# Optimization experiments

Hardware: AMD Instinct MI355X
Metric: run time of the kernel (lower is better)

## Reference

```python
import jax, jax.numpy as jnp
import numpy as np

B, N, IN_DIM = 256, 300, 1280
DIM, DEPTH, HEADS = 256, 2, 4
DIM_HEAD = DIM // HEADS            # 64
NB_FEAT = int(DIM_HEAD * np.log(DIM_HEAD))  # 266, lucidrains default
FF_HIDDEN = 4 * DIM
LN_EPS = 1e-5
KERNEL_EPS = 1e-4


def _orthogonal_random_matrix(nb_rows, nb_cols, rng):
    # gaussian orthogonal random matrix, scaling=0 (chi-norm multipliers)
    blocks = []
    full = nb_rows // nb_cols
    for _ in range(full):
        q, _ = np.linalg.qr(rng.standard_normal((nb_cols, nb_cols)))
        blocks.append(q.T)
    rem = nb_rows - full * nb_cols
    if rem:
        q, _ = np.linalg.qr(rng.standard_normal((nb_cols, nb_cols)))
        blocks.append(q.T[:rem])
    mat = np.concatenate(blocks, 0)
    mult = np.linalg.norm(rng.standard_normal((nb_rows, nb_cols)), axis=1)
    return (mult[:, None] * mat).astype(np.float32)


def setup_inputs() -> dict:
    key = jax.random.key(0)
    ks = jax.random.split(key, 24)
    s = 0.02
    rng = np.random.default_rng(0)
    proj = jnp.asarray(np.stack([_orthogonal_random_matrix(NB_FEAT, DIM_HEAD, rng)
                                 for _ in range(DEPTH)]))  # [L, M, dh]
    return {
        "x": jax.random.normal(ks[0], (B, N, IN_DIM), jnp.float32),
        "w_in": jax.random.normal(ks[1], (IN_DIM, DIM), jnp.float32) * s,
        "b_in": jnp.zeros((DIM,), jnp.float32),
        "proj": proj,
        "ln1_g": jnp.ones((DEPTH, DIM), jnp.float32),
        "ln1_b": jnp.zeros((DEPTH, DIM), jnp.float32),
        "wq": jax.random.normal(ks[2], (DEPTH, DIM, DIM), jnp.float32) * s,
        "wk": jax.random.normal(ks[3], (DEPTH, DIM, DIM), jnp.float32) * s,
        "wv": jax.random.normal(ks[4], (DEPTH, DIM, DIM), jnp.float32) * s,
        "wo": jax.random.normal(ks[5], (DEPTH, DIM, DIM), jnp.float32) * s,
        "bo": jnp.zeros((DEPTH, DIM), jnp.float32),
        "ln2_g": jnp.ones((DEPTH, DIM), jnp.float32),
        "ln2_b": jnp.zeros((DEPTH, DIM), jnp.float32),
        "w1": jax.random.normal(ks[6], (DEPTH, DIM, FF_HIDDEN), jnp.float32) * s,
        "b1": jnp.zeros((DEPTH, FF_HIDDEN), jnp.float32),
        "w2": jax.random.normal(ks[7], (DEPTH, FF_HIDDEN, DIM), jnp.float32) * s,
        "b2": jnp.zeros((DEPTH, DIM), jnp.float32),
        "hln_g": jnp.ones((DIM,), jnp.float32),
        "hln_b": jnp.zeros((DIM,), jnp.float32),
        "wh1": jax.random.normal(ks[8], (DIM, 128), jnp.float32) * s,
        "bh1": jnp.zeros((128,), jnp.float32),
        "wh2": jax.random.normal(ks[9], (128, 1), jnp.float32) * s,
        "bh2": jnp.zeros((1,), jnp.float32),
    }


def _layernorm(x, g, b):
    mu = jnp.mean(x, -1, keepdims=True)
    var = jnp.mean(jnp.square(x - mu), -1, keepdims=True)
    return (x - mu) * jax.lax.rsqrt(var + LN_EPS) * g + b


def _softmax_kernel(data, proj, is_query):
    # data: [b,h,n,dh], proj: [m,dh] -> features [b,h,n,m] (FAVOR+ positive softmax kernel)
    norm = DIM_HEAD ** -0.25
    ratio = proj.shape[0] ** -0.5
    dd = jnp.einsum('bhnd,md->bhnm', data * norm, proj)
    diag = 0.5 * jnp.sum(jnp.square(data), -1) * (norm ** 2)  # [b,h,n]
    if is_query:
        stab = jnp.max(dd, axis=-1, keepdims=True)
    else:
        stab = jnp.max(dd, axis=(-2, -1), keepdims=True)
    return ratio * (jnp.exp(dd - diag[..., None] - stab) + KERNEL_EPS)


def _linear_attention(q, k, v, proj):
    # non-causal FAVOR+: O(n*m*d) instead of O(n^2*d)
    qp = _softmax_kernel(q, proj, True)    # [b,h,n,m]
    kp = _softmax_kernel(k, proj, False)   # [b,h,n,m]
    d_inv = 1.0 / jnp.einsum('bhnm,bhm->bhn', qp, jnp.sum(kp, axis=-2))
    context = jnp.einsum('bhnm,bhnd->bhmd', kp, v)
    return jnp.einsum('bhnm,bhmd->bhnd', qp, context) * d_inv[..., None]


def reference(x, w_in, b_in, proj, ln1_g, ln1_b, wq, wk, wv, wo, bo,
              ln2_g, ln2_b, w1, b1, w2, b2, hln_g, hln_b, wh1, bh1, wh2, bh2):
    h = x @ w_in + b_in                                   # [B,N,DIM]
    for l in range(DEPTH):
        # --- pre-norm FAVOR+ self-attention ---
        y = _layernorm(h, ln1_g[l], ln1_b[l])
        q = (y @ wq[l]).reshape(B, N, HEADS, DIM_HEAD).transpose(0, 2, 1, 3)
        k = (y @ wk[l]).reshape(B, N, HEADS, DIM_HEAD).transpose(0, 2, 1, 3)
        v = (y @ wv[l]).reshape(B, N, HEADS, DIM_HEAD).transpose(0, 2, 1, 3)
        o = _linear_attention(q, k, v, proj[l])
        o = o.transpose(0, 2, 1, 3).reshape(B, N, DIM)
        h = h + (o @ wo[l] + bo[l])
        # --- pre-norm FFN (GELU, mult=4) ---
        y = _layernorm(h, ln2_g[l], ln2_b[l])
        h = h + (jax.nn.gelu(y @ w1[l] + b1[l]) @ w2[l] + b2[l])
    pooled = jnp.mean(h, axis=1)                          # [B,DIM]
    z = _layernorm(pooled, hln_g, hln_b)
    z = jax.nn.relu(z @ wh1 + bh1)
    return jax.nn.sigmoid(z @ wh2 + bh2)                  # [B,1]
```

## Files before the change

kernel.cpp:

```cpp
#include <hip/hip_runtime.h>
#include <hip/hip_bf16.h>


#define MF 266
#define NSEQ 300
#define DIMC 256
#define NORM_QK 0.3535533905932738f
#define KEPS 1e-4f

typedef __attribute__((ext_vector_type(8))) short bf16x8;
typedef __attribute__((ext_vector_type(4))) float f32x4;

#define MFMA16(a, b, c) __builtin_amdgcn_mfma_f32_16x16x32_bf16((a), (b), (c), 0, 0, 0)

__device__ __forceinline__ float bfbits2f(ushort u) {
  return __uint_as_float(((unsigned int)u) << 16);
}
__device__ __forceinline__ ushort f2us(float f) {
  __hip_bfloat16 b = __float2bfloat16(f);
  return *(ushort*)&b;
}
__device__ __forceinline__ float sq8(uint4 u) {
  float s = 0.f;
  const unsigned int uu[4] = {u.x, u.y, u.z, u.w};
#pragma unroll
  for (int i = 0; i < 4; i++) {
    const float a = bfbits2f((ushort)(uu[i] & 0xffff));
    const float b = bfbits2f((ushort)(uu[i] >> 16));
    s += a * a + b * b;
  }
  return s;
}
__device__ __forceinline__ void gld16(const void* g, void* l) {
  __builtin_amdgcn_global_load_lds(
      (const __attribute__((address_space(1))) unsigned int*)g,
      (__attribute__((address_space(3))) unsigned int*)l, 16, 0, 0);
}
__device__ __forceinline__ float fast_gelu(float x) {
  const float t = 0.7978845608028654f * (x + 0.044715f * x * x * x);
  const float e = __expf(2.0f * fabsf(t));
  float th = 1.0f - 2.0f / (e + 1.0f);
  th = (t < 0.0f) ? -th : th;
  return 0.5f * x * (1.0f + th);
}

template<int EPI, int OUTBF, int AF32>
__global__ __launch_bounds__(256) void gemm_mfma(
    const ushort* __restrict__ A, const float* __restrict__ Af,
    const ushort* __restrict__ BT,
    const float* __restrict__ bias, const float* __restrict__ R,
    float* __restrict__ Cf, __hip_bfloat16* __restrict__ Cb,
    ushort* __restrict__ Cq, int M, int N, int K)
{
  __shared__ ushort As[128][32];
  __shared__ ushort Bs[128][32];
  const int tid = threadIdx.x;
  const int row0 = blockIdx.y << 7, col0 = blockIdx.x << 7;
  const int w = tid >> 6, lane = tid & 63;
  const int wm = (w >> 1) << 6, wn = (w & 1) << 6;
  const int r = lane & 15, quad = lane >> 4;
  const int sr = tid >> 2, sc = (tid & 3) << 3;
  f32x4 acc[4][4];
#pragma unroll
  for (int i = 0; i < 4; i++)
#pragma unroll
    for (int j = 0; j < 4; j++) acc[i][j] = (f32x4){0.f, 0.f, 0.f, 0.f};
  const ushort* ap0 = A + (size_t)(row0 + sr) * K + sc;
  const ushort* ap1 = A + (size_t)(row0 + sr + 64) * K + sc;
  const float*  af0 = Af + (size_t)(row0 + sr) * K + sc;
  const float*  af1 = Af + (size_t)(row0 + sr + 64) * K + sc;
  const ushort* bp0 = BT + (size_t)(col0 + sr) * K + sc;
  const ushort* bp1 = BT + (size_t)(col0 + sr + 64) * K + sc;
  for (int k0 = 0; k0 < K; k0 += 32) {
    if (AF32) {
      const float4 u0 = *(const float4*)(af0 + k0);
      const float4 u1 = *(const float4*)(af0 + k0 + 4);
      const float4 u2 = *(const float4*)(af1 + k0);
      const float4 u3 = *(const float4*)(af1 + k0 + 4);
      ushort4 p0, p1, p2, p3;
      p0.x=f2us(u0.x); p0.y=f2us(u0.y); p0.z=f2us(u0.z); p0.w=f2us(u0.w);
      p1.x=f2us(u1.x); p1.y=f2us(u1.y); p1.z=f2us(u1.z); p1.w=f2us(u1.w);
      p2.x=f2us(u2.x); p2.y=f2us(u2.y); p2.z=f2us(u2.z); p2.w=f2us(u2.w);
      p3.x=f2us(u3.x); p3.y=f2us(u3.y); p3.z=f2us(u3.z); p3.w=f2us(u3.w);
      *(ushort4*)&As[sr][sc]      = p0;
      *(ushort4*)&As[sr][sc+4]    = p1;
      *(ushort4*)&As[sr+64][sc]   = p2;
      *(ushort4*)&As[sr+64][sc+4] = p3;
    } else {
      gld16(ap0 + k0, &As[sr][sc]);
      gld16(ap1 + k0, &As[sr + 64][sc]);
    }
    gld16(bp0 + k0, &Bs[sr][sc]);
    gld16(bp1 + k0, &Bs[sr + 64][sc]);
    __syncthreads();
    bf16x8 af[4], bfv[4];
#pragma unroll
    for (int i = 0; i < 4; i++) af[i]  = *(const bf16x8*)&As[wm + i*16 + r][quad << 3];
#pragma unroll
    for (int i = 0; i < 4; i++) bfv[i] = *(const bf16x8*)&Bs[wn + i*16 + r][quad << 3];
#pragma unroll
    for (int mi = 0; mi < 4; mi++)
#pragma unroll
      for (int ni = 0; ni < 4; ni++)
        acc[mi][ni] = MFMA16(af[mi], bfv[ni], acc[mi][ni]);
    __syncthreads();
  }
#pragma unroll
  for (int mi = 0; mi < 4; mi++) {
    const int rowb = row0 + wm + mi*16 + (quad << 2);
#pragma unroll
    for (int ni = 0; ni < 4; ni++) {
      const int col = col0 + wn + ni*16 + r;
      if (EPI == 4) {
        const int tsel = col >> 8, hd = col & 255, hh = hd >> 6, d = hd & 63;
        const float sc_ = (tsel == 2) ? 1.f : NORM_QK;
#pragma unroll
        for (int j = 0; j < 4; j++) {
          const int rowj = rowb + j;
          const int bq = rowj / 300, nq = rowj - bq * 300;
          Cq[(((size_t)tsel * 1024 + (bq << 2) + hh) * 300 + nq) * 64 + d] =
              f2us(acc[mi][ni][j] * sc_);
        }
      } else {
        const float bv = bias[col];
#pragma unroll
        for (int j = 0; j < 4; j++) {
          const size_t off = (size_t)(rowb + j) * N + col;
          float vv = acc[mi][ni][j] + bv;
          if (EPI == 1) vv += R[off];
          if (OUTBF) Cb[off] = __float2bfloat16(vv);
          else       Cf[off] = vv;
        }
      }
    }
  }
}

__global__ __launch_bounds__(256) void pack_ffn(
    const ushort* __restrict__ w1T, const ushort* __restrict__ w2T,
    const ushort* __restrict__ woT,
    ushort* __restrict__ W1P, ushort* __restrict__ W2P,
    ushort* __restrict__ WOP)
{
  const int c = blockIdx.x * 256 + threadIdx.x;
  if (c < 32768) {
    const int l = c & 63, g = c >> 6;
    const int r = l & 15, q = l >> 4;
    const int nc = g >> 6, w = (g >> 3) & 7, ks = g & 7;
    *(uint4*)(W1P + (size_t)c * 8) =
        *(const uint4*)(w1T + (size_t)(nc*128 + w*16 + r) * 256 + ks*32 + q*8);
  } else if (c < 65536) {
    const int ci = c - 32768;
    const int l = ci & 63, g = ci >> 6;
    const int r = l & 15, q = l >> 4;
    const int nc = g >> 6, w = (g >> 3) & 7, kq = (g >> 1) & 3, jn = g & 1;
    *(uint4*)(W2P + (size_t)ci * 8) =
        *(const uint4*)(w2T + (size_t)(w*32 + jn*16 + r) * 1024 + nc*128 + kq*32 + q*8);
  } else {
    const int ci = c - 65536;
    const int l = ci & 63, g = ci >> 6;
    const int r = l & 15, q = l >> 4;
    const int ks = g >> 4, nt = g & 15;
    *(uint4*)(WOP + (size_t)ci * 8) =
        *(const uint4*)(woT + (size_t)(nt*16 + r) * 256 + ks*32 + q*8);
  }
}

__global__ __launch_bounds__(512, 6) void aoffn_kernel(
    float* __restrict__ h, const ushort* __restrict__ ob,
    const ushort* __restrict__ WOP, const float* __restrict__ bo,
    const ushort* __restrict__ W1P, const float* __restrict__ b1,
    const ushort* __restrict__ W2P, const float* __restrict__ b2,
    const float* __restrict__ lng, const float* __restrict__ lnb)
{
  __shared__ ushort Ys[64][264];
  __shared__ ushort Hs[64][136];
  __shared__ float red1[64][2], red2[64][2];
  const int tid = threadIdx.x, w = tid >> 6, lane = tid & 63;
  const int r = lane & 15, quad = lane >> 4;
  const int row0 = blockIdx.x << 6;

  {
    const ushort* obp = ob + (size_t)row0 * DIMC;
#pragma unroll
    for (int p = 0; p < 4; p++) {
      const int i = tid + p*512;
      const int rr = i >> 5, cc = (i & 31) << 3;
      *(uint4*)&Ys[rr][cc] = *(const uint4*)(obp + rr*DIMC + cc);
    }
  }
  __syncthreads();

  const int mt = w & 3, nh = w >> 2;
  f32x4 wacc[8];
#pragma unroll
  for (int i = 0; i < 8; i++) wacc[i] = (f32x4){0.f, 0.f, 0.f, 0.f};
  {
    const ushort* wop = WOP + ((size_t)(nh*8) * 64 + lane) * 8;
#pragma unroll
    for (int ks = 0; ks < 8; ks++) {
      const bf16x8 a = *(const bf16x8*)&Ys[mt*16 + r][ks*32 + (quad << 3)];
#pragma unroll
      for (int nt = 0; nt < 8; nt++) {
        const bf16x8 bb = *(const bf16x8*)(wop + ((size_t)ks*16 + nt) * 512);
        wacc[nt] = MFMA16(a, bb, wacc[nt]);
      }
    }
  }
  {
    float s1[4] = {0.f,0.f,0.f,0.f}, s2[4] = {0.f,0.f,0.f,0.f};
#pragma unroll
    for (int nt = 0; nt < 8; nt++) {
      const int col = (nh << 7) + nt*16 + r;
      const float bv = bo[col];
#pragma unroll
      for (int j = 0; j < 4; j++) {
        const int rowj = mt*16 + (quad << 2) + j;
        const float hn = wacc[nt][j] + bv + h[(size_t)(row0 + rowj)*DIMC + col];
        wacc[nt][j] = hn;
        s1[j] += hn; s2[j] += hn*hn;
      }
    }
#pragma unroll
    for (int off = 1; off < 16; off <<= 1)
#pragma unroll
      for (int j = 0; j < 4; j++) {
        s1[j] += __shfl_xor(s1[j], off);
        s2[j] += __shfl_xor(s2[j], off);
      }
    if (r == 0) {
#pragma unroll
      for (int j = 0; j < 4; j++) {
        const int rowj = mt*16 + (quad << 2) + j;
        red1[rowj][nh] = s1[j];
        red2[rowj][nh] = s2[j];
      }
    }
  }
  __syncthreads();
  {
    float mu[4], rstd[4];
#pragma unroll
    for (int j = 0; j < 4; j++) {
      const int rowj = mt*16 + (quad << 2) + j;
      mu[j] = (red1[rowj][0] + red1[rowj][1]) * (1.0f/256.0f);
      const float e2 = (red2[rowj][0] + red2[rowj][1]) * (1.0f/256.0f);
      rstd[j] = rsqrtf(e2 - mu[j]*mu[j] + 1e-5f);
    }
#pragma unroll
    for (int nt = 0; nt < 8; nt++) {
      const int col = (nh << 7) + nt*16 + r;
      const float gg = lng[col], bb = lnb[col];
#pragma unroll
      for (int j = 0; j < 4; j++) {
        const int rowj = mt*16 + (quad << 2) + j;
        const float hn = wacc[nt][j];
        h[(size_t)(row0 + rowj)*DIMC + col] = hn;
        Ys[rowj][col] = f2us((hn - mu[j]) * rstd[j] * gg + bb);
      }
    }
  }
  __syncthreads();

  f32x4 oacc[4][2];
#pragma unroll
  for (int i = 0; i < 4; i++)
#pragma unroll
    for (int j = 0; j < 2; j++) oacc[i][j] = (f32x4){0.f, 0.f, 0.f, 0.f};

#pragma unroll 1
  for (int nc = 0; nc < 8; nc++) {
    f32x4 hacc[4];
#pragma unroll
    for (int i = 0; i < 4; i++) hacc[i] = (f32x4){0.f, 0.f, 0.f, 0.f};
    const ushort* w1p = W1P + ((size_t)((nc*8 + w) * 8) * 64 + lane) * 8;
#pragma unroll
    for (int ks = 0; ks < 8; ks++) {
      const bf16x8 a = *(const bf16x8*)(w1p + ks * 512);
#pragma unroll
      for (int mj = 0; mj < 4; mj++) {
        const bf16x8 y = *(const bf16x8*)&Ys[mj*16 + r][ks*32 + (quad << 3)];
        hacc[mj] = MFMA16(a, y, hacc[mj]);
      }
    }
    const int khb = (w << 4) + (quad << 2);
    const float4 bv = *(const float4*)(b1 + nc*128 + khb);
#pragma unroll
    for (int mj = 0; mj < 4; mj++) {
      ushort4 hv;
      hv.x = f2us(fast_gelu(hacc[mj][0] + bv.x));
      hv.y = f2us(fast_gelu(hacc[mj][1] + bv.y));
      hv.z = f2us(fast_gelu(hacc[mj][2] + bv.z));
      hv.w = f2us(fast_gelu(hacc[mj][3] + bv.w));
      *(ushort4*)&Hs[mj*16 + r][khb] = hv;
    }
    __syncthreads();
    const ushort* w2p = W2P + ((size_t)((nc*8 + w) * 8) * 64 + lane) * 8;
#pragma unroll
    for (int kq = 0; kq < 4; kq++) {
      bf16x8 hf[4];
#pragma unroll
      for (int mi = 0; mi < 4; mi++)
        hf[mi] = *(const bf16x8*)&Hs[mi*16 + r][kq*32 + (quad << 3)];
#pragma unroll
      for (int jn = 0; jn < 2; jn++) {
        const bf16x8 bb = *(const bf16x8*)(w2p + (kq*2 + jn) * 512);
#pragma unroll
        for (int mi = 0; mi < 4; mi++)
          oacc[mi][jn] = MFMA16(hf[mi], bb, oacc[mi][jn]);
      }
    }
    __syncthreads();
  }

#pragma unroll
  for (int mi = 0; mi < 4; mi++) {
    const int mbase = row0 + mi*16 + (quad << 2);
#pragma unroll
    for (int jn = 0; jn < 2; jn++) {
      const int n = (w << 5) + jn*16 + r;
      const float b2v = b2[n];
#pragma unroll
      for (int jj = 0; jj < 4; jj++) {
        float* hp = h + (size_t)(mbase + jj) * DIMC + n;
        *hp += oacc[mi][jn][jj] + b2v;
      }
    }
  }
}

__global__ __launch_bounds__(256) void cast_bf16_kernel(
    const float* __restrict__ in, ushort* __restrict__ out, int n4)
{
  const int i = blockIdx.x * 256 + threadIdx.x;
  if (i >= n4) return;
  const float4 v = ((const float4*)in)[i];
  ushort4 rr;
  rr.x = f2us(v.x); rr.y = f2us(v.y); rr.z = f2us(v.z); rr.w = f2us(v.w);
  ((ushort4*)out)[i] = rr;
}

struct TSeg { const float* src; ushort* dst; int R; int C; int base; };
struct TTab { TSeg s[13]; };
__global__ __launch_bounds__(256) void tcast_all(TTab tab) {
  __shared__ float t[32][33];
  const int bid = blockIdx.x;
  int si = 0;
#pragma unroll
  for (int i = 1; i < 13; i++) if (bid >= tab.s[i].base) si = i;
  const float* src = tab.s[si].src;
  ushort* dst = tab.s[si].dst;
  const int R = tab.s[si].R, C = tab.s[si].C;
  const int local = bid - tab.s[si].base;
  const int cw = C >> 5;
  const int c0 = (local % cw) << 5, r0 = (local / cw) << 5;
  const int tx = threadIdx.x & 31, ty = threadIdx.x >> 5;
#pragma unroll
  for (int i = 0; i < 32; i += 8)
    t[ty + i][tx] = src[(size_t)(r0 + ty + i) * C + c0 + tx];
  __syncthreads();
#pragma unroll
  for (int i = 0; i < 32; i += 8)
    dst[(size_t)(c0 + ty + i) * R + r0 + tx] = f2us(t[tx][ty + i]);
}

__global__ __launch_bounds__(256) void ln_kernel(
    const float* __restrict__ x, const float* __restrict__ g,
    const float* __restrict__ b, __hip_bfloat16* __restrict__ y)
{
  const int wid = threadIdx.x >> 6, lane = threadIdx.x & 63;
  const int row = blockIdx.x * 4 + wid;
  const float* xr = x + (size_t)row * DIMC;
  float v[4];
  float s = 0.f;
#pragma unroll
  for (int i = 0; i < 4; i++) { v[i] = xr[lane + 64*i]; s += v[i]; }
#pragma unroll
  for (int off = 32; off; off >>= 1) s += __shfl_xor(s, off);
  const float mu = s * (1.0f/256.0f);
  float var = 0.f;
#pragma unroll
  for (int i = 0; i < 4; i++) { const float d = v[i] - mu; var += d*d; }
#pragma unroll
  for (int off = 32; off; off >>= 1) var += __shfl_xor(var, off);
  const float rstd = rsqrtf(var * (1.0f/256.0f) + 1e-5f);
  __hip_bfloat16* yr = y + (size_t)row * DIMC;
#pragma unroll
  for (int i = 0; i < 4; i++) {
    const int c = lane + 64*i;
    yr[c] = __float2bfloat16((v[i] - mu) * rstd * g[c] + b[c]);
  }
}

__global__ __launch_bounds__(512) void favor_fused_kernel(
    const ushort* __restrict__ qn_all, const ushort* __restrict__ kn_all,
    const ushort* __restrict__ v_all, const ushort* __restrict__ projb,
    ushort* __restrict__ Ob)
{
  __shared__ __align__(16) uint8_t smem[151424];
  ushort (*kn_s)[72]      = (ushort(*)[72])(smem);
  ushort (*vT_s)[328]     = (ushort(*)[328])(smem + 46080);
  ushort (*proj_s)[72]    = (ushort(*)[72])(smem + 88064);
  ushort (*kpT_s)[40]     = (ushort(*)[40])(smem + 127232);
  ushort (*qp_s)[16][72]  = (ushort(*)[16][72])(smem + 127232);
  float* diag_s = (float*)(smem + 148992);
  float* ksum_s = (float*)(smem + 150272);
  float* red_s  = (float*)(smem + 151360);

  const int tid = threadIdx.x, w = tid >> 6, lane = tid & 63;
  const int bh = blockIdx.x;
  const int b = bh >> 2, h = bh & 3;
  const int r = lane & 15, quad = lane >> 4;
  const int rl = lane >> 3, c8 = lane & 7;

  {
    const ushort* knb = kn_all + (size_t)bh * 19200;
    for (int row = w*8 + rl; row < 320; row += 64) {
      uint4 u = {0u,0u,0u,0u};
      if (row < 300) u = *(const uint4*)(knb + row*64 + c8*8);
      *(uint4*)&kn_s[row][c8*8] = u;
      float s = sq8(u);
      s += __shfl_xor(s, 1); s += __shfl_xor(s, 2); s += __shfl_xor(s, 4);
      if (c8 == 0) diag_s[row] = 0.5f * s;
    }
    const ushort* vb = v_all + (size_t)bh * 19200;
    for (int row = w*8 + rl; row < 328; row += 64) {
      uint4 u = {0u,0u,0u,0u};
      if (row < 300) u = *(const uint4*)(vb + row*64 + c8*8);
      const unsigned int uu[4] = {u.x, u.y, u.z, u.w};
#pragma unroll
      for (int p = 0; p < 4; p++) {
        vT_s[c8*8 + 2*p    ][row] = (ushort)(uu[p] & 0xffff);
        vT_s[c8*8 + 2*p + 1][row] = (ushort)(uu[p] >> 16);
      }
    }
    for (int row = w*8 + rl; row < 272; row += 64) {
      uint4 u = {0u,0u,0u,0u};
      if (row < 266) u = *(const uint4*)(projb + row*64 + c8*8);
      *(uint4*)&proj_s[row][c8*8] = u;
    }
  }
  __syncthreads();

  f32x4 cacc[9];
#pragma unroll
  for (int i = 0; i < 9; i++) cacc[i] = (f32x4){0.f,0.f,0.f,0.f};
  float ksum_acc = 0.f;
  float stab = -3.0e38f;

#pragma unroll 1
  for (int c = 0; c < 10; c++) {
    f32x4 ddreg[5];
    float cmax = -3.0e38f;
#pragma unroll
    for (int ii = 0; ii < 5; ii++) {
      const int t = w + ii*8;
      if (t < 34) {
        const int tm = t >> 1, tn = c*2 + (t & 1);
        const bf16x8 a0 = *(const bf16x8*)&proj_s[tm*16 + r][quad*8];
        const bf16x8 a1 = *(const bf16x8*)&proj_s[tm*16 + r][32 + quad*8];
        const bf16x8 b0 = *(const bf16x8*)&kn_s[tn*16 + r][quad*8];
        const bf16x8 b1 = *(const bf16x8*)&kn_s[tn*16 + r][32 + quad*8];
        f32x4 acc = (f32x4){0.f,0.f,0.f,0.f};
        acc = MFMA16(a0, b0, acc);
        acc = MFMA16(a1, b1, acc);
        ddreg[ii] = acc;
        const int n = tn*16 + r;
        if (n < 300) {
#pragma unroll
          for (int j = 0; j < 4; j++) {
            const int m = tm*16 + quad*4 + j;
            if (m < 266) cmax = fmaxf(cmax, acc[j]);
          }
        }
      }
    }
#pragma unroll
    for (int off = 32; off; off >>= 1) cmax = fmaxf(cmax, __shfl_xor(cmax, off));
    if (lane == 0) red_s[w] = cmax;
    __syncthreads();
    float bmax = red_s[0];
#pragma unroll
    for (int i = 1; i < 8; i++) bmax = fmaxf(bmax, red_s[i]);
    const float stab_new = fmaxf(stab, bmax);
    const float alpha = __expf(stab - stab_new);
    stab = stab_new;
    ksum_acc *= alpha;
#pragma unroll
    for (int i = 0; i < 9; i++)
#pragma unroll
      for (int j = 0; j < 4; j++) cacc[i][j] *= alpha;
#pragma unroll
    for (int ii = 0; ii < 5; ii++) {
      const int t = w + ii*8;
      if (t < 34) {
        const int tm = t >> 1, tnl = t & 1, tn = c*2 + tnl;
        const int n = tn*16 + r;
        const float dgn = diag_s[n];
#pragma unroll
        for (int j = 0; j < 4; j++) {
          const int m = tm*16 + quad*4 + j;
          float kp = 0.f;
          if (n < 300 && m < 266) kp = __expf(ddreg[ii][j] - dgn - stab) + KEPS;
          kpT_s[m][tnl*16 + r] = f2us(kp);
        }
      }
    }
    __syncthreads();
    if (tid < 272) {
      float rs = 0.f;
#pragma unroll
      for (int kk = 0; kk < 4; kk++) {
        const uint4 u = *(const uint4*)&kpT_s[tid][kk*8];
        const unsigned int uu[4] = {u.x, u.y, u.z, u.w};
#pragma unroll
        for (int p = 0; p < 4; p++)
          rs += bfbits2f((ushort)(uu[p] & 0xffff)) + bfbits2f((ushort)(uu[p] >> 16));
      }
      ksum_acc += rs;
    }
#pragma unroll
    for (int ii = 0; ii < 9; ii++) {
      const int t2 = w + ii*8;
      if (t2 < 68) {
        const int tm = t2 >> 2, td = t2 & 3;
        const bf16x8 aa = *(const bf16x8*)&kpT_s[tm*16 + r][quad*8];
        const bf16x8 bb = *(const bf16x8*)&vT_s[td*16 + r][c*32 + quad*8];
        cacc[ii] = MFMA16(aa, bb, cacc[ii]);
      }
    }
    __syncthreads();
  }

  if (tid < 272) ksum_s[tid] = ksum_acc;
#pragma unroll
  for (int ii = 0; ii < 9; ii++) {
    const int t2 = w + ii*8;
    if (t2 < 68) {
      const int tm = t2 >> 2, td = t2 & 3;
#pragma unroll
      for (int j = 0; j < 4; j++) {
        const int m = tm*16 + quad*4 + j;
        vT_s[td*16 + r][m] = f2us(cacc[ii][j]);
      }
    }
  }
  {
    const ushort* qb = qn_all + (size_t)bh * 19200;
    for (int row = w*8 + rl; row < 320; row += 64) {
      uint4 u = {0u,0u,0u,0u};
      if (row < 300) u = *(const uint4*)(qb + row*64 + c8*8);
      *(uint4*)&kn_s[row][c8*8] = u;
      float s = sq8(u);
      s += __shfl_xor(s, 1); s += __shfl_xor(s, 2); s += __shfl_xor(s, 4);
      if (c8 == 0) diag_s[row] = 0.5f * s;
    }
  }
  __syncthreads();

#pragma unroll 1
  for (int t = w; t < 19; t += 8) {
    const bf16x8 a0 = *(const bf16x8*)&kn_s[t*16 + r][quad*8];
    const bf16x8 a1 = *(const bf16x8*)&kn_s[t*16 + r][32 + quad*8];
    f32x4 dd[17];
#pragma unroll
    for (int tm = 0; tm < 17; tm++) {
      const bf16x8 b0 = *(const bf16x8*)&proj_s[tm*16 + r][quad*8];
      const bf16x8 b1 = *(const bf16x8*)&proj_s[tm*16 + r][32 + quad*8];
      f32x4 acc = (f32x4){0.f,0.f,0.f,0.f};
      acc = MFMA16(a0, b0, acc);
      acc = MFMA16(a1, b1, acc);
      dd[tm] = acc;
    }
    float mxj[4] = {-3.0e38f, -3.0e38f, -3.0e38f, -3.0e38f};
#pragma unroll
    for (int tm = 0; tm < 17; tm++) {
      if (tm*16 + r < 266) {
#pragma unroll
        for (int j = 0; j < 4; j++) mxj[j] = fmaxf(mxj[j], dd[tm][j]);
      }
    }
#pragma unroll
    for (int off = 1; off < 16; off <<= 1)
#pragma unroll
      for (int j = 0; j < 4; j++) mxj[j] = fmaxf(mxj[j], __shfl_xor(mxj[j], off));
    float dg[4];
#pragma unroll
    for (int j = 0; j < 4; j++) dg[j] = diag_s[t*16 + quad*4 + j];
    float den[4] = {0.f, 0.f, 0.f, 0.f};
#pragma unroll
    for (int tm = 0; tm < 17; tm++) {
      const float ks = ksum_s[tm*16 + r];
      const bool mval = (tm*16 + r < 266);
#pragma unroll
      for (int j = 0; j < 4; j++) {
        const int n = t*16 + quad*4 + j;
        float qp = 0.f;
        if (mval && n < 300) qp = __expf(dd[tm][j] - dg[j] - mxj[j]) + KEPS;
        dd[tm][j] = qp;
        den[j] += qp * ks;
      }
    }
#pragma unroll
    for (int off = 1; off < 16; off <<= 1)
#pragma unroll
      for (int j = 0; j < 4; j++) den[j] += __shfl_xor(den[j], off);
    float dinv[4];
#pragma unroll
    for (int j = 0; j < 4; j++) dinv[j] = 1.0f / den[j];

    f32x4 oacc[4];
#pragma unroll
    for (int td = 0; td < 4; td++) oacc[td] = (f32x4){0.f,0.f,0.f,0.f};
#pragma unroll
    for (int g = 0; g < 5; g++) {
#pragma unroll
      for (int tt = 0; tt < 4; tt++) {
        const int tm = g*4 + tt;
#pragma unroll
        for (int j = 0; j < 4; j++) {
          const ushort us = (tm <= 16) ? f2us(dd[tm][j]) : (ushort)0;
          qp_s[w][quad*4 + j][tt*16 + r] = us;
        }
      }
#pragma unroll
      for (int s = 0; s < 2; s++) {
        const bf16x8 aa = *(const bf16x8*)&qp_s[w][r][s*32 + quad*8];
#pragma unroll
        for (int td = 0; td < 4; td++) {
          const bf16x8 bb = *(const bf16x8*)&vT_s[td*16 + r][g*64 + s*32 + quad*8];
          oacc[td] = MFMA16(aa, bb, oacc[td]);
        }
      }
    }
#pragma unroll
    for (int td = 0; td < 4; td++) {
#pragma unroll
      for (int j = 0; j < 4; j++) {
        const int n = t*16 + quad*4 + j;
        if (n < 300)
          Ob[((size_t)b*300 + n)*256 + h*64 + td*16 + r] = f2us(oacc[td][j] * dinv[j]);
      }
    }
  }
}

__global__ __launch_bounds__(256) void head_kernel(
    const float* __restrict__ h, const float* __restrict__ hg,
    const float* __restrict__ hb, const float* __restrict__ wh1,
    const float* __restrict__ bh1, const float* __restrict__ wh2,
    const float* __restrict__ bh2, float* __restrict__ out)
{
  __shared__ float z_s[256];
  __shared__ float hid_s[128];
  __shared__ float red_s[4];
  const int b = blockIdx.x, tid = threadIdx.x;
  const float* hb_ = h + (size_t)b * NSEQ * DIMC;
  float s = 0.f;
  for (int n = 0; n < NSEQ; n++) s += hb_[(size_t)n * DIMC + tid];
  s *= (1.0f / 300.0f);
  float t1 = s;
#pragma unroll
  for (int off = 32; off; off >>= 1) t1 += __shfl_xor(t1, off);
  if ((tid & 63) == 0) red_s[tid >> 6] = t1;
  __syncthreads();
  const float mu = (red_s[0] + red_s[1] + red_s[2] + red_s[3]) * (1.0f/256.0f);
  __syncthreads();
  const float d = s - mu;
  float vv = d * d;
#pragma unroll
  for (int off = 32; off; off >>= 1) vv += __shfl_xor(vv, off);
  if ((tid & 63) == 0) red_s[tid >> 6] = vv;
  __syncthreads();
  const float var = (red_s[0] + red_s[1] + red_s[2] + red_s[3]) * (1.0f/256.0f);
  z_s[tid] = d * rsqrtf(var + 1e-5f) * hg[tid] + hb[tid];
  __syncthreads();
  if (tid < 128) {
    float acc = bh1[tid];
    for (int dd = 0; dd < 256; dd++) acc += z_s[dd] * wh1[dd * 128 + tid];
    hid_s[tid] = fmaxf(acc, 0.f);
  }
  __syncthreads();
  if (tid < 64) {
    float acc = hid_s[tid] * wh2[tid] + hid_s[tid + 64] * wh2[tid + 64];
#pragma unroll
    for (int off = 32; off; off >>= 1) acc += __shfl_xor(acc, off);
    if (tid == 0) {
      const float val = acc + bh2[0];
      out[b] = 1.0f / (1.0f + __expf(-val));
    }
  }
}

extern "C" void kernel_launch(void* const* d_in, const int* in_sizes, int n_in,
                              void* d_out, int out_size, void* d_ws, size_t ws_size,
                              hipStream_t stream) {
  const float* x    = (const float*)d_in[0];
  const float* w_in = (const float*)d_in[1];
  const float* b_in = (const float*)d_in[2];
  const float* proj = (const float*)d_in[3];
  const float* ln1g = (const float*)d_in[4];
  const float* ln1b = (const float*)d_in[5];
  const float* wq   = (const float*)d_in[6];
  const float* wk   = (const float*)d_in[7];
  const float* wv   = (const float*)d_in[8];
  const float* wo   = (const float*)d_in[9];
  const float* bo   = (const float*)d_in[10];
  const float* ln2g = (const float*)d_in[11];
  const float* ln2b = (const float*)d_in[12];
  const float* w1   = (const float*)d_in[13];
  const float* b1   = (const float*)d_in[14];
  const float* w2   = (const float*)d_in[15];
  const float* b2   = (const float*)d_in[16];
  const float* hg   = (const float*)d_in[17];
  const float* hbp  = (const float*)d_in[18];
  const float* wh1  = (const float*)d_in[19];
  const float* bh1  = (const float*)d_in[20];
  const float* wh2  = (const float*)d_in[21];
  const float* bh2  = (const float*)d_in[22];

  uint8_t* base = (uint8_t*)d_ws;
  float*  h     = (float*)(base);
  ushort* yb    = (ushort*)(base + 78643200);
  ushort* qkv   = (ushort*)(base + 117964800);
  ushort* ob    = (ushort*)(base + 235929600);
  ushort* wbuf  = (ushort*)(base + 275251200);
  ushort* projb = (ushort*)(base + 279052288);
  ushort* wopb  = (ushort*)(base + 279120384);
  ushort* qb = qkv;
  ushort* kb = qkv + 19660800;
  ushort* vb = qkv + 39321600;
  ushort* scr = qkv;

  ushort* w_inT = wbuf;
  ushort* wT0   = wbuf + 327680;

  cast_bf16_kernel<<<34, 256, 0, stream>>>(proj, projb, 8512);
  TTab tab;
  int nb = 0;
  {
    int idx = 0, basem = 0;
    auto seg = [&](const float* s, ushort* d, int R, int C) {
      tab.s[idx] = TSeg{s, d, R, C, basem};
      basem += (R >> 5) * (C >> 5);
      idx++;
    };
    seg(w_in, w_inT, 1280, 256);
    for (int l = 0; l < 2; l++) {
      ushort* wl = wT0 + (size_t)l * 786432;
      seg(wq + (size_t)l*65536,  wl,          256, 256);
      seg(wk + (size_t)l*65536,  wl + 65536,  256, 256);
      seg(wv + (size_t)l*65536,  wl + 131072, 256, 256);
      seg(wo + (size_t)l*65536,  wl + 196608, 256, 256);
      seg(w1 + (size_t)l*262144, scr + (size_t)l*524288,          256, 1024);
      seg(w2 + (size_t)l*262144, scr + (size_t)l*524288 + 262144, 1024, 256);
    }
    nb = basem;
  }
  tcast_all<<<nb, 256, 0, stream>>>(tab);
  for (int l = 0; l < 2; l++) {
    ushort* wl = wT0 + (size_t)l * 786432;
    pack_ffn<<<288, 256, 0, stream>>>(
        scr + (size_t)l*524288, scr + (size_t)l*524288 + 262144,
        wl + 196608,
        wl + 262144, wl + 524288, wopb + (size_t)l*65536);
  }

  gemm_mfma<0,0,1><<<dim3(2, 600), 256, 0, stream>>>(
      nullptr, x, w_inT, b_in, nullptr, h, nullptr, nullptr, 76800, 256, 1280);

  for (int l = 0; l < 2; l++) {
    ushort* wl = wT0 + (size_t)l * 786432;
    ushort* projL = projb + (size_t)l * 17024;
    ln_kernel<<<19200, 256, 0, stream>>>(h, ln1g + l*256, ln1b + l*256, (__hip_bfloat16*)yb);
    gemm_mfma<4,0,0><<<dim3(6, 600), 256, 0, stream>>>(
        yb, nullptr, wl, nullptr, nullptr, nullptr, nullptr, qkv, 76800, 768, 256);
    favor_fused_kernel<<<1024, 512, 0, stream>>>(qb, kb, vb, projL, ob);
    aoffn_kernel<<<1200, 512, 0, stream>>>(
        h, ob, wopb + (size_t)l*65536, bo + l*256,
        wl + 262144, b1 + (size_t)l*1024, wl + 524288, b2 + (size_t)l*256,
        ln2g + l*256, ln2b + l*256);
  }
  head_kernel<<<256, 256, 0, stream>>>(h, hg, hbp, wh1, bh1, wh2, bh2, (float*)d_out);
}
```

Before: 1.570 ms.

## Split fused FAVOR kernel into K-side and Q-side kernels with MFMA-packed operands

The single FAVOR+ attention kernel used about 148KB of LDS, which limited it to one block per CU. It is replaced by two kernels. The K-side kernel builds the context and ksum and writes them to global memory; the Q-side kernel reads them back and computes the output. The QKV GEMM epilogue now writes Q and K directly in the MFMA fragment layout, and the projection matrix is pre-packed the same way, so fragments are loaded straight from global memory and never staged through LDS. This allows smaller shared memory and more resident blocks, at the cost of an extra launch and a global round-trip for the context.

```diff
diff --git a/kernel.cpp b/kernel.cpp
--- a/kernel.cpp
+++ b/kernel.cpp
@@ -50,7 +50,8 @@
     const ushort* __restrict__ BT,
     const float* __restrict__ bias, const float* __restrict__ R,
     float* __restrict__ Cf, __hip_bfloat16* __restrict__ Cb,
-    ushort* __restrict__ Cq, int M, int N, int K)
+    ushort* __restrict__ Cq, ushort* __restrict__ Qpk, ushort* __restrict__ Kpk,
+    int M, int N, int K)
 {
   __shared__ ushort As[128][32];
   __shared__ ushort Bs[128][32];
@@ -113,13 +114,20 @@
       const int col = col0 + wn + ni*16 + r;
       if (EPI == 4) {
         const int tsel = col >> 8, hd = col & 255, hh = hd >> 6, d = hd & 63;
-        const float sc_ = (tsel == 2) ? 1.f : NORM_QK;
 #pragma unroll
         for (int j = 0; j < 4; j++) {
           const int rowj = rowb + j;
           const int bq = rowj / 300, nq = rowj - bq * 300;
-          Cq[(((size_t)tsel * 1024 + (bq << 2) + hh) * 300 + nq) * 64 + d] =
-              f2us(acc[mi][ni][j] * sc_);
+          const int bh = (bq << 2) + hh;
+          if (tsel == 2) {
+            Cq[((size_t)bh * 300 + nq) * 64 + d] = f2us(acc[mi][ni][j]);
+          } else {
+            const int t = nq >> 4, rr = nq & 15;
+            const int kh = d >> 5, qq = (d >> 3) & 3, off = d & 7;
+            ushort* dst = (tsel == 0) ? Qpk : Kpk;
+            dst[((size_t)((bh * 20 + t) * 2 + kh)) * 512 + (qq * 16 + rr) * 8 + off] =
+                f2us(acc[mi][ni][j] * NORM_QK);
+          }
         }
       } else {
         const float bv = bias[col];
@@ -138,11 +146,12 @@
 
 __global__ __launch_bounds__(256) void pack_ffn(
     const ushort* __restrict__ w1T, const ushort* __restrict__ w2T,
-    const ushort* __restrict__ woT,
+    const ushort* __restrict__ woT, const ushort* __restrict__ projbL,
     ushort* __restrict__ W1P, ushort* __restrict__ W2P,
-    ushort* __restrict__ WOP)
+    ushort* __restrict__ WOP, ushort* __restrict__ PROJPK)
 {
   const int c = blockIdx.x * 256 + threadIdx.x;
+  if (c >= 75904) return;
   if (c < 32768) {
     const int l = c & 63, g = c >> 6;
     const int r = l & 15, q = l >> 4;
@@ -156,13 +165,274 @@
     const int nc = g >> 6, w = (g >> 3) & 7, kq = (g >> 1) & 3, jn = g & 1;
     *(uint4*)(W2P + (size_t)ci * 8) =
         *(const uint4*)(w2T + (size_t)(w*32 + jn*16 + r) * 1024 + nc*128 + kq*32 + q*8);
-  } else {
+  } else if (c < 73728) {
     const int ci = c - 65536;
     const int l = ci & 63, g = ci >> 6;
     const int r = l & 15, q = l >> 4;
     const int ks = g >> 4, nt = g & 15;
     *(uint4*)(WOP + (size_t)ci * 8) =
         *(const uint4*)(woT + (size_t)(nt*16 + r) * 256 + ks*32 + q*8);
+  } else {
+    const int ci = c - 73728;
+    const int l = ci & 63, g = ci >> 6;
+    const int tm = g >> 1, kh = g & 1;
+    const int row = tm*16 + (l & 15), col = kh*32 + (l >> 4)*8;
+    uint4 u = {0u,0u,0u,0u};
+    if (row < 266) u = *(const uint4*)(projbL + (size_t)row*64 + col);
+    *(uint4*)(PROJPK + (size_t)g * 512 + l * 8) = u;
+  }
+}
+
+__global__ __launch_bounds__(512, 4) void favor_k_kernel(
+    const ushort* __restrict__ kpk, const ushort* __restrict__ v_all,
+    const ushort* __restrict__ projpk,
+    ushort* __restrict__ ctxg, float* __restrict__ ksumg)
+{
+  __shared__ ushort vT_s[64][328];
+  __shared__ ushort kpT_s[272][40];
+  __shared__ float diag_s[320];
+  __shared__ float red_s[8];
+  const int tid = threadIdx.x, w = tid >> 6, lane = tid & 63;
+  const int bh = blockIdx.x;
+  const int r = lane & 15, quad = lane >> 4;
+  const int rl = lane >> 3, c8 = lane & 7;
+
+  for (int t = w; t < 19; t += 8) {
+    const ushort* kp0 = kpk + ((size_t)(bh*20 + t) * 2) * 512 + lane * 8;
+    float s = sq8(*(const uint4*)kp0) + sq8(*(const uint4*)(kp0 + 512));
+    s += __shfl_xor(s, 16); s += __shfl_xor(s, 32);
+    if (lane < 16) diag_s[t*16 + lane] = 0.5f * s;
+  }
+  {
+    const ushort* vb = v_all + (size_t)bh * 19200;
+    for (int row = w*8 + rl; row < 328; row += 64) {
+      uint4 u = {0u,0u,0u,0u};
+      if (row < 300) u = *(const uint4*)(vb + row*64 + c8*8);
+      const unsigned int uu[4] = {u.x, u.y, u.z, u.w};
+#pragma unroll
+      for (int p = 0; p < 4; p++) {
+        vT_s[c8*8 + 2*p    ][row] = (ushort)(uu[p] & 0xffff);
+        vT_s[c8*8 + 2*p + 1][row] = (ushort)(uu[p] >> 16);
+      }
+    }
+  }
+  __syncthreads();
+
+  f32x4 cacc[9];
+#pragma unroll
+  for (int i = 0; i < 9; i++) cacc[i] = (f32x4){0.f,0.f,0.f,0.f};
+  float ksum_acc = 0.f;
+  float stab = -3.0e38f;
+
+#pragma unroll 1
+  for (int c = 0; c < 10; c++) {
+    f32x4 ddreg[5];
+    float cmax = -3.0e38f;
+#pragma unroll
+    for (int ii = 0; ii < 5; ii++) {
+      const int t = w + ii*8;
+      if (t < 34) {
+        const int tm = t >> 1, tn = c*2 + (t & 1);
+        const ushort* pf = projpk + (size_t)(tm * 2) * 512 + lane * 8;
+        const ushort* kf = kpk + ((size_t)(bh*20 + tn) * 2) * 512 + lane * 8;
+        const bf16x8 a0 = *(const bf16x8*)pf;
+        const bf16x8 a1 = *(const bf16x8*)(pf + 512);
+        const bf16x8 b0 = *(const bf16x8*)kf;
+        const bf16x8 b1 = *(const bf16x8*)(kf + 512);
+        f32x4 acc = (f32x4){0.f,0.f,0.f,0.f};
+        acc = MFMA16(a0, b0, acc);
+        acc = MFMA16(a1, b1, acc);
+        ddreg[ii] = acc;
+        const int n = tn*16 + r;
+        if (n < 300) {
+#pragma unroll
+          for (int j = 0; j < 4; j++) {
+            const int m = tm*16 + quad*4 + j;
+            if (m < 266) cmax = fmaxf(cmax, acc[j]);
+          }
+        }
+      }
+    }
+#pragma unroll
+    for (int off = 32; off; off >>= 1) cmax = fmaxf(cmax, __shfl_xor(cmax, off));
+    if (lane == 0) red_s[w] = cmax;
+    __syncthreads();
+    float bmax = red_s[0];
+#pragma unroll
+    for (int i = 1; i < 8; i++) bmax = fmaxf(bmax, red_s[i]);
+    const float stab_new = fmaxf(stab, bmax);
+    const float alpha = __expf(stab - stab_new);
+    stab = stab_new;
+    ksum_acc *= alpha;
+#pragma unroll
+    for (int i = 0; i < 9; i++)
+#pragma unroll
+      for (int j = 0; j < 4; j++) cacc[i][j] *= alpha;
+#pragma unroll
+    for (int ii = 0; ii < 5; ii++) {
+      const int t = w + ii*8;
+      if (t < 34) {
+        const int tm = t >> 1, tnl = t & 1, tn = c*2 + tnl;
+        const int n = tn*16 + r;
+        const float dgn = diag_s[n & 319];
+#pragma unroll
+        for (int j = 0; j < 4; j++) {
+          const int m = tm*16 + quad*4 + j;
+          float kp = 0.f;
+          if (n < 300 && m < 266) kp = __expf(ddreg[ii][j] - dgn - stab) + KEPS;
+          kpT_s[m][tnl*16 + r] = f2us(kp);
+        }
+      }
+    }
+    __syncthreads();
+    if (tid < 272) {
+      float rs = 0.f;
+#pragma unroll
+      for (int kk = 0; kk < 4; kk++) {
+        const uint4 u = *(const uint4*)&kpT_s[tid][kk*8];
+        const unsigned int uu[4] = {u.x, u.y, u.z, u.w};
+#pragma unroll
+        for (int p = 0; p < 4; p++)
+          rs += bfbits2f((ushort)(uu[p] & 0xffff)) + bfbits2f((ushort)(uu[p] >> 16));
+      }
+      ksum_acc += rs;
+    }
+#pragma unroll
+    for (int ii = 0; ii < 9; ii++) {
+      const int t2 = w + ii*8;
+      if (t2 < 68) {
+        const int tm = t2 >> 2, td = t2 & 3;
+        const bf16x8 aa = *(const bf16x8*)&kpT_s[tm*16 + r][quad*8];
+        const bf16x8 bb = *(const bf16x8*)&vT_s[td*16 + r][c*32 + quad*8];
+        cacc[ii] = MFMA16(aa, bb, cacc[ii]);
+      }
+    }
+    __syncthreads();
+  }
+
+  if (tid < 272) ksumg[(size_t)bh * 272 + tid] = ksum_acc;
+#pragma unroll
+  for (int ii = 0; ii < 9; ii++) {
+    const int t2 = w + ii*8;
+    if (t2 < 68) {
+      const int tm = t2 >> 2, td = t2 & 3;
+#pragma unroll
+      for (int j = 0; j < 4; j++) {
+        const int m = tm*16 + quad*4 + j;
+        ctxg[(size_t)bh * 20480 + (td*16 + r) * 320 + m] = f2us(cacc[ii][j]);
+      }
+    }
+  }
+}
+
+__global__ __launch_bounds__(512, 4) void favor_q_kernel(
+    const ushort* __restrict__ qpk, const ushort* __restrict__ projpk,
+    const ushort* __restrict__ ctxg, const float* __restrict__ ksumg,
+    ushort* __restrict__ Ob)
+{
+  __shared__ ushort ctx_s[64][328];
+  __shared__ ushort qp_s[8][16][72];
+  __shared__ float diag_s[320];
+  __shared__ float ksum_s[272];
+  const int tid = threadIdx.x, w = tid >> 6, lane = tid & 63;
+  const int bh = blockIdx.x;
+  const int b = bh >> 2, h = bh & 3;
+  const int r = lane & 15, quad = lane >> 4;
+
+  for (int i = tid; i < 2560; i += 512) {
+    const int rr = i / 40, cc = i - rr * 40;
+    uint4 u = {0u,0u,0u,0u};
+    if (cc < 34) u = *(const uint4*)(ctxg + (size_t)bh*20480 + rr*320 + cc*8);
+    *(uint4*)&ctx_s[rr][cc*8] = u;
+  }
+  if (tid < 272) ksum_s[tid] = ksumg[(size_t)bh * 272 + tid];
+  for (int t = w; t < 19; t += 8) {
+    const ushort* qp0 = qpk + ((size_t)(bh*20 + t) * 2) * 512 + lane * 8;
+    float s = sq8(*(const uint4*)qp0) + sq8(*(const uint4*)(qp0 + 512));
+    s += __shfl_xor(s, 16); s += __shfl_xor(s, 32);
+    if (lane < 16) diag_s[t*16 + lane] = 0.5f * s;
+  }
+  __syncthreads();
+
+#pragma unroll 1
+  for (int t = w; t < 19; t += 8) {
+    const ushort* qf = qpk + ((size_t)(bh*20 + t) * 2) * 512 + lane * 8;
+    const bf16x8 a0 = *(const bf16x8*)qf;
+    const bf16x8 a1 = *(const bf16x8*)(qf + 512);
+    float mxj[4] = {-3.0e38f, -3.0e38f, -3.0e38f, -3.0e38f};
+#pragma unroll
+    for (int tm = 0; tm < 17; tm++) {
+      const ushort* pf = projpk + (size_t)(tm * 2) * 512 + lane * 8;
+      f32x4 acc = (f32x4){0.f,0.f,0.f,0.f};
+      acc = MFMA16(a0, *(const bf16x8*)pf, acc);
+      acc = MFMA16(a1, *(const bf16x8*)(pf + 512), acc);
+      if (tm*16 + r < 266) {
+#pragma unroll
+        for (int j = 0; j < 4; j++) mxj[j] = fmaxf(mxj[j], acc[j]);
+      }
+    }
+#pragma unroll
+    for (int off = 1; off < 16; off <<= 1)
+#pragma unroll
+      for (int j = 0; j < 4; j++) mxj[j] = fmaxf(mxj[j], __shfl_xor(mxj[j], off));
+    float dg[4];
+#pragma unroll
+    for (int j = 0; j < 4; j++) dg[j] = diag_s[t*16 + quad*4 + j];
+    float den[4] = {0.f, 0.f, 0.f, 0.f};
+    f32x4 oacc[4];
+#pragma unroll
+    for (int td = 0; td < 4; td++) oacc[td] = (f32x4){0.f,0.f,0.f,0.f};
+#pragma unroll
+    for (int g = 0; g < 5; g++) {
+#pragma unroll
+      for (int tt = 0; tt < 4; tt++) {
+        const int tm = g*4 + tt;
+        if (tm <= 16) {
+          const ushort* pf = projpk + (size_t)(tm * 2) * 512 + lane * 8;
+          f32x4 acc = (f32x4){0.f,0.f,0.f,0.f};
+          acc = MFMA16(a0, *(const bf16x8*)pf, acc);
+          acc = MFMA16(a1, *(const bf16x8*)(pf + 512), acc);
+          const float ks = ksum_s[tm*16 + r];
+          const bool mval = (tm*16 + r < 266);
+#pragma unroll
+          for (int j = 0; j < 4; j++) {
+            const int n = t*16 + quad*4 + j;
+            float qp = 0.f;
+            if (mval && n < 300) qp = __expf(acc[j] - dg[j] - mxj[j]) + KEPS;
+            den[j] += qp * ks;
+            qp_s[w][quad*4 + j][tt*16 + r] = f2us(qp);
+          }
+        } else {
+#pragma unroll
+          for (int j = 0; j < 4; j++) qp_s[w][quad*4 + j][tt*16 + r] = 0;
+        }
+      }
+#pragma unroll
+      for (int s = 0; s < 2; s++) {
+        const bf16x8 aa = *(const bf16x8*)&qp_s[w][r][s*32 + quad*8];
+#pragma unroll
+        for (int td = 0; td < 4; td++) {
+          const bf16x8 bb = *(const bf16x8*)&ctx_s[td*16 + r][g*64 + s*32 + quad*8];
+          oacc[td] = MFMA16(aa, bb, oacc[td]);
+        }
+      }
+    }
+#pragma unroll
+    for (int off = 1; off < 16; off <<= 1)
+#pragma unroll
+      for (int j = 0; j < 4; j++) den[j] += __shfl_xor(den[j], off);
+    float dinv[4];
+#pragma unroll
+    for (int j = 0; j < 4; j++) dinv[j] = 1.0f / den[j];
+#pragma unroll
+    for (int td = 0; td < 4; td++) {
+#pragma unroll
+      for (int j = 0; j < 4; j++) {
+        const int n = t*16 + quad*4 + j;
+        if (n < 300)
+          Ob[((size_t)b*300 + n)*256 + h*64 + td*16 + r] = f2us(oacc[td][j] * dinv[j]);
+      }
+    }
   }
 }
 
@@ -389,259 +659,6 @@
   for (int i = 0; i < 4; i++) {
     const int c = lane + 64*i;
     yr[c] = __float2bfloat16((v[i] - mu) * rstd * g[c] + b[c]);
-  }
-}
-
-__global__ __launch_bounds__(512) void favor_fused_kernel(
-    const ushort* __restrict__ qn_all, const ushort* __restrict__ kn_all,
-    const ushort* __restrict__ v_all, const ushort* __restrict__ projb,
-    ushort* __restrict__ Ob)
-{
-  __shared__ __align__(16) uint8_t smem[151424];
-  ushort (*kn_s)[72]      = (ushort(*)[72])(smem);
-  ushort (*vT_s)[328]     = (ushort(*)[328])(smem + 46080);
-  ushort (*proj_s)[72]    = (ushort(*)[72])(smem + 88064);
-  ushort (*kpT_s)[40]     = (ushort(*)[40])(smem + 127232);
-  ushort (*qp_s)[16][72]  = (ushort(*)[16][72])(smem + 127232);
-  float* diag_s = (float*)(smem + 148992);
-  float* ksum_s = (float*)(smem + 150272);
-  float* red_s  = (float*)(smem + 151360);
-
-  const int tid = threadIdx.x, w = tid >> 6, lane = tid & 63;
-  const int bh = blockIdx.x;
-  const int b = bh >> 2, h = bh & 3;
-  const int r = lane & 15, quad = lane >> 4;
-  const int rl = lane >> 3, c8 = lane & 7;
-
-  {
-    const ushort* knb = kn_all + (size_t)bh * 19200;
-    for (int row = w*8 + rl; row < 320; row += 64) {
-      uint4 u = {0u,0u,0u,0u};
-      if (row < 300) u = *(const uint4*)(knb + row*64 + c8*8);
-      *(uint4*)&kn_s[row][c8*8] = u;
-      float s = sq8(u);
-      s += __shfl_xor(s, 1); s += __shfl_xor(s, 2); s += __shfl_xor(s, 4);
-      if (c8 == 0) diag_s[row] = 0.5f * s;
-    }
-    const ushort* vb = v_all + (size_t)bh * 19200;
-    for (int row = w*8 + rl; row < 328; row += 64) {
-      uint4 u = {0u,0u,0u,0u};
-      if (row < 300) u = *(const uint4*)(vb + row*64 + c8*8);
-      const unsigned int uu[4] = {u.x, u.y, u.z, u.w};
-#pragma unroll
-      for (int p = 0; p < 4; p++) {
-        vT_s[c8*8 + 2*p    ][row] = (ushort)(uu[p] & 0xffff);
-        vT_s[c8*8 + 2*p + 1][row] = (ushort)(uu[p] >> 16);
-      }
-    }
-    for (int row = w*8 + rl; row < 272; row += 64) {
-      uint4 u = {0u,0u,0u,0u};
-      if (row < 266) u = *(const uint4*)(projb + row*64 + c8*8);
-      *(uint4*)&proj_s[row][c8*8] = u;
-    }
-  }
-  __syncthreads();
-
-  f32x4 cacc[9];
-#pragma unroll
-  for (int i = 0; i < 9; i++) cacc[i] = (f32x4){0.f,0.f,0.f,0.f};
-  float ksum_acc = 0.f;
-  float stab = -3.0e38f;
-
-#pragma unroll 1
-  for (int c = 0; c < 10; c++) {
-    f32x4 ddreg[5];
-    float cmax = -3.0e38f;
-#pragma unroll
-    for (int ii = 0; ii < 5; ii++) {
-      const int t = w + ii*8;
-      if (t < 34) {
-        const int tm = t >> 1, tn = c*2 + (t & 1);
-        const bf16x8 a0 = *(const bf16x8*)&proj_s[tm*16 + r][quad*8];
-        const bf16x8 a1 = *(const bf16x8*)&proj_s[tm*16 + r][32 + quad*8];
-        const bf16x8 b0 = *(const bf16x8*)&kn_s[tn*16 + r][quad*8];
-        const bf16x8 b1 = *(const bf16x8*)&kn_s[tn*16 + r][32 + quad*8];
-        f32x4 acc = (f32x4){0.f,0.f,0.f,0.f};
-        acc = MFMA16(a0, b0, acc);
-        acc = MFMA16(a1, b1, acc);
-        ddreg[ii] = acc;
-        const int n = tn*16 + r;
-        if (n < 300) {
-#pragma unroll
-          for (int j = 0; j < 4; j++) {
-            const int m = tm*16 + quad*4 + j;
-            if (m < 266) cmax = fmaxf(cmax, acc[j]);
-          }
-        }
-      }
-    }
-#pragma unroll
-    for (int off = 32; off; off >>= 1) cmax = fmaxf(cmax, __shfl_xor(cmax, off));
-    if (lane == 0) red_s[w] = cmax;
-    __syncthreads();
-    float bmax = red_s[0];
-#pragma unroll
-    for (int i = 1; i < 8; i++) bmax = fmaxf(bmax, red_s[i]);
-    const float stab_new = fmaxf(stab, bmax);
-    const float alpha = __expf(stab - stab_new);
-    stab = stab_new;
-    ksum_acc *= alpha;
-#pragma unroll
-    for (int i = 0; i < 9; i++)
-#pragma unroll
-      for (int j = 0; j < 4; j++) cacc[i][j] *= alpha;
-#pragma unroll
-    for (int ii = 0; ii < 5; ii++) {
-      const int t = w + ii*8;
-      if (t < 34) {
-        const int tm = t >> 1, tnl = t & 1, tn = c*2 + tnl;
-        const int n = tn*16 + r;
-        const float dgn = diag_s[n];
-#pragma unroll
-        for (int j = 0; j < 4; j++) {
-          const int m = tm*16 + quad*4 + j;
-          float kp = 0.f;
-          if (n < 300 && m < 266) kp = __expf(ddreg[ii][j] - dgn - stab) + KEPS;
-          kpT_s[m][tnl*16 + r] = f2us(kp);
-        }
-      }
-    }
-    __syncthreads();
-    if (tid < 272) {
-      float rs = 0.f;
-#pragma unroll
-      for (int kk = 0; kk < 4; kk++) {
-        const uint4 u = *(const uint4*)&kpT_s[tid][kk*8];
-        const unsigned int uu[4] = {u.x, u.y, u.z, u.w};
-#pragma unroll
-        for (int p = 0; p < 4; p++)
-          rs += bfbits2f((ushort)(uu[p] & 0xffff)) + bfbits2f((ushort)(uu[p] >> 16));
-      }
-      ksum_acc += rs;
-    }
-#pragma unroll
-    for (int ii = 0; ii < 9; ii++) {
-      const int t2 = w + ii*8;
-      if (t2 < 68) {
-        const int tm = t2 >> 2, td = t2 & 3;
-        const bf16x8 aa = *(const bf16x8*)&kpT_s[tm*16 + r][quad*8];
-        const bf16x8 bb = *(const bf16x8*)&vT_s[td*16 + r][c*32 + quad*8];
-        cacc[ii] = MFMA16(aa, bb, cacc[ii]);
-      }
-    }
-    __syncthreads();
-  }
-
-  if (tid < 272) ksum_s[tid] = ksum_acc;
-#pragma unroll
-  for (int ii = 0; ii < 9; ii++) {
-    const int t2 = w + ii*8;
-    if (t2 < 68) {
-      const int tm = t2 >> 2, td = t2 & 3;
-#pragma unroll
-      for (int j = 0; j < 4; j++) {
-        const int m = tm*16 + quad*4 + j;
-        vT_s[td*16 + r][m] = f2us(cacc[ii][j]);
-      }
-    }
-  }
-  {
-    const ushort* qb = qn_all + (size_t)bh * 19200;
-    for (int row = w*8 + rl; row < 320; row += 64) {
-      uint4 u = {0u,0u,0u,0u};
-      if (row < 300) u = *(const uint4*)(qb + row*64 + c8*8);
-      *(uint4*)&kn_s[row][c8*8] = u;
-      float s = sq8(u);
-      s += __shfl_xor(s, 1); s += __shfl_xor(s, 2); s += __shfl_xor(s, 4);
-      if (c8 == 0) diag_s[row] = 0.5f * s;
-    }
-  }
-  __syncthreads();
-
-#pragma unroll 1
-  for (int t = w; t < 19; t += 8) {
-    const bf16x8 a0 = *(const bf16x8*)&kn_s[t*16 + r][quad*8];
-    const bf16x8 a1 = *(const bf16x8*)&kn_s[t*16 + r][32 + quad*8];
-    f32x4 dd[17];
-#pragma unroll
-    for (int tm = 0; tm < 17; tm++) {
-      const bf16x8 b0 = *(const bf16x8*)&proj_s[tm*16 + r][quad*8];
-      const bf16x8 b1 = *(const bf16x8*)&proj_s[tm*16 + r][32 + quad*8];
-      f32x4 acc = (f32x4){0.f,0.f,0.f,0.f};
-      acc = MFMA16(a0, b0, acc);
-      acc = MFMA16(a1, b1, acc);
-      dd[tm] = acc;
-    }
-    float mxj[4] = {-3.0e38f, -3.0e38f, -3.0e38f, -3.0e38f};
-#pragma unroll
-    for (int tm = 0; tm < 17; tm++) {
-      if (tm*16 + r < 266) {
-#pragma unroll
-        for (int j = 0; j < 4; j++) mxj[j] = fmaxf(mxj[j], dd[tm][j]);
-      }
-    }
-#pragma unroll
-    for (int off = 1; off < 16; off <<= 1)
-#pragma unroll
-      for (int j = 0; j < 4; j++) mxj[j] = fmaxf(mxj[j], __shfl_xor(mxj[j], off));
-    float dg[4];
-#pragma unroll
-    for (int j = 0; j < 4; j++) dg[j] = diag_s[t*16 + quad*4 + j];
-    float den[4] = {0.f, 0.f, 0.f, 0.f};
-#pragma unroll
-    for (int tm = 0; tm < 17; tm++) {
-      const float ks = ksum_s[tm*16 + r];
-      const bool mval = (tm*16 + r < 266);
-#pragma unroll
-      for (int j = 0; j < 4; j++) {
-        const int n = t*16 + quad*4 + j;
-        float qp = 0.f;
-        if (mval && n < 300) qp = __expf(dd[tm][j] - dg[j] - mxj[j]) + KEPS;
-        dd[tm][j] = qp;
-        den[j] += qp * ks;
-      }
-    }
-#pragma unroll
-    for (int off = 1; off < 16; off <<= 1)
-#pragma unroll
-      for (int j = 0; j < 4; j++) den[j] += __shfl_xor(den[j], off);
-    float dinv[4];
-#pragma unroll
-    for (int j = 0; j < 4; j++) dinv[j] = 1.0f / den[j];
-
-    f32x4 oacc[4];
-#pragma unroll
-    for (int td = 0; td < 4; td++) oacc[td] = (f32x4){0.f,0.f,0.f,0.f};
-#pragma unroll
-    for (int g = 0; g < 5; g++) {
-#pragma unroll
-      for (int tt = 0; tt < 4; tt++) {
-        const int tm = g*4 + tt;
-#pragma unroll
-        for (int j = 0; j < 4; j++) {
-          const ushort us = (tm <= 16) ? f2us(dd[tm][j]) : (ushort)0;
-          qp_s[w][quad*4 + j][tt*16 + r] = us;
-        }
-      }
-#pragma unroll
-      for (int s = 0; s < 2; s++) {
-        const bf16x8 aa = *(const bf16x8*)&qp_s[w][r][s*32 + quad*8];
-#pragma unroll
-        for (int td = 0; td < 4; td++) {
-          const bf16x8 bb = *(const bf16x8*)&vT_s[td*16 + r][g*64 + s*32 + quad*8];
-          oacc[td] = MFMA16(aa, bb, oacc[td]);
-        }
-      }
-    }
-#pragma unroll
-    for (int td = 0; td < 4; td++) {
-#pragma unroll
-      for (int j = 0; j < 4; j++) {
-        const int n = t*16 + quad*4 + j;
-        if (n < 300)
-          Ob[((size_t)b*300 + n)*256 + h*64 + td*16 + r] = f2us(oacc[td][j] * dinv[j]);
-      }
-    }
   }
 }
 
@@ -722,15 +739,17 @@
   uint8_t* base = (uint8_t*)d_ws;
   float*  h     = (float*)(base);
   ushort* yb    = (ushort*)(base + 78643200);
-  ushort* qkv   = (ushort*)(base + 117964800);
-  ushort* ob    = (ushort*)(base + 235929600);
-  ushort* wbuf  = (ushort*)(base + 275251200);
-  ushort* projb = (ushort*)(base + 279052288);
-  ushort* wopb  = (ushort*)(base + 279120384);
-  ushort* qb = qkv;
-  ushort* kb = qkv + 19660800;
-  ushort* vb = qkv + 39321600;
-  ushort* scr = qkv;
+  ushort* vb    = (ushort*)(base + 117964800);
+  ushort* qpk   = (ushort*)(base + 157286400);
+  ushort* kpk   = (ushort*)(base + 199229440);
+  ushort* ob    = (ushort*)(base + 241172480);
+  ushort* ctxg  = (ushort*)(base + 280494080);
+  float*  ksumg = (float*) (base + 322437120);
+  ushort* wbuf  = (ushort*)(base + 323551232);
+  ushort* projb = (ushort*)(base + 327352320);
+  ushort* wopb  = (ushort*)(base + 327420416);
+  ushort* projpk= (ushort*)(base + 327682560);
+  ushort* scr = qpk;
 
   ushort* w_inT = wbuf;
   ushort* wT0   = wbuf + 327680;
@@ -760,22 +779,26 @@
   tcast_all<<<nb, 256, 0, stream>>>(tab);
   for (int l = 0; l < 2; l++) {
     ushort* wl = wT0 + (size_t)l * 786432;
-    pack_ffn<<<288, 256, 0, stream>>>(
+    pack_ffn<<<297, 256, 0, stream>>>(
         scr + (size_t)l*524288, scr + (size_t)l*524288 + 262144,
-        wl + 196608,
-        wl + 262144, wl + 524288, wopb + (size_t)l*65536);
+        wl + 196608, projb + (size_t)l*17024,
+        wl + 262144, wl + 524288, wopb + (size_t)l*65536,
+        projpk + (size_t)l*17408);
   }
 
   gemm_mfma<0,0,1><<<dim3(2, 600), 256, 0, stream>>>(
-      nullptr, x, w_inT, b_in, nullptr, h, nullptr, nullptr, 76800, 256, 1280);
+      nullptr, x, w_inT, b_in, nullptr, h, nullptr, nullptr, nullptr, nullptr,
+      76800, 256, 1280);
 
   for (int l = 0; l < 2; l++) {
     ushort* wl = wT0 + (size_t)l * 786432;
-    ushort* projL = projb + (size_t)l * 17024;
+    ushort* projpkL = projpk + (size_t)l * 17408;
     ln_kernel<<<19200, 256, 0, stream>>>(h, ln1g + l*256, ln1b + l*256, (__hip_bfloat16*)yb);
     gemm_mfma<4,0,0><<<dim3(6, 600), 256, 0, stream>>>(
-        yb, nullptr, wl, nullptr, nullptr, nullptr, nullptr, qkv, 76800, 768, 256);
-    favor_fused_kernel<<<1024, 512, 0, stream>>>(qb, kb, vb, projL, ob);
+        yb, nullptr, wl, nullptr, nullptr, nullptr, nullptr, vb, qpk, kpk,
+        76800, 768, 256);
+    favor_k_kernel<<<1024, 512, 0, stream>>>(kpk, vb, projpkL, ctxg, ksumg);
+    favor_q_kernel<<<1024, 512, 0, stream>>>(qpk, projpkL, ctxg, ksumg, ob);
     aoffn_kernel<<<1200, 512, 0, stream>>>(
         h, ob, wopb + (size_t)l*65536, bo + l*256,
         wl + 262144, b1 + (size_t)l*1024, wl + 524288, b2 + (size_t)l*256,
```

Result: slower. 2.037 ms (+29.8%).
